# Performance work log

Hardware: AMD Instinct MI355X
Metric: run time of the kernel (lower is better)

## Reference

```python
import math
import jax, jax.numpy as jnp
import numpy as np

N, QLEN, KLEN, DMODEL, NHEAD = 2, 2048, 2048, 1024, 16
DK = DMODEL // NHEAD
MY_INF = 1000000000000.0


def setup_inputs() -> dict:
    key = jax.random.key(0)
    ks = jax.random.split(key, 12)
    s = 1.0 / math.sqrt(DMODEL)
    return {
        "q": jax.random.normal(ks[0], (N, QLEN, DMODEL), jnp.float32),
        "k": jax.random.normal(ks[1], (N, KLEN, DMODEL), jnp.float32),
        "v": jax.random.normal(ks[2], (N, KLEN, DMODEL), jnp.float32),
        "mask": jax.random.randint(ks[3], (N, 1, QLEN, KLEN), 0, 2) > 0,
        "Wq": jax.random.uniform(ks[4], (DMODEL, DMODEL), jnp.float32, -s, s),
        "bq": jnp.zeros((DMODEL,), jnp.float32),
        "Wk": jax.random.uniform(ks[5], (DMODEL, DMODEL), jnp.float32, -s, s),
        "bk": jnp.zeros((DMODEL,), jnp.float32),
        "Wv": jax.random.uniform(ks[6], (DMODEL, DMODEL), jnp.float32, -s, s),
        "bv": jnp.zeros((DMODEL,), jnp.float32),
        "Wo": jax.random.uniform(ks[7], (DMODEL, DMODEL), jnp.float32, -s, s),
        "bo": jnp.zeros((DMODEL,), jnp.float32),
    }


def _mha(q, k, v, mask, Wq, bq, Wk, bk, Wv, bv, Wo, bo):
    n, q_len, _ = q.shape
    k_len = k.shape[1]
    # QKV projections, split into heads: [n, H, len, d_k]
    q_ = (q @ Wq.T + bq).reshape(n, q_len, NHEAD, DK).transpose(0, 2, 1, 3)
    k_ = (k @ Wk.T + bk).reshape(n, k_len, NHEAD, DK).transpose(0, 2, 1, 3)
    v_ = (v @ Wv.T + bv).reshape(n, k_len, NHEAD, DK).transpose(0, 2, 1, 3)
    # scores: [n, H, q_len, k_len]
    scores = jnp.einsum("nhqd,nhkd->nhqk", q_, k_) / math.sqrt(DK)
    scores = jnp.where(mask, -MY_INF, scores)
    attn = jax.nn.softmax(scores, axis=-1)
    ctx = jnp.einsum("nhqk,nhkd->nhqd", attn, v_)
    concat = ctx.transpose(0, 2, 1, 3).reshape(n, q_len, DMODEL)
    # dropout is identity in eval mode
    return concat @ Wo.T + bo


def reference(q, k, v, mask, Wq, bq, Wk, bk, Wv, bv, Wo, bo):
    return _mha(q, k, v, mask, Wq, bq, Wk, bk, Wv, bv, Wo, bo)
```

## Files before the change

kernel.cpp:

```cpp
#include <hip/hip_runtime.h>
#include <hip/hip_bf16.h>
#include <stdint.h>

typedef unsigned short u16;
typedef unsigned long long u64;
typedef __attribute__((ext_vector_type(8))) short bf16x8;
typedef __attribute__((ext_vector_type(4))) float f32x4;

#define DMODEL 1024
#define NHEAD  16
#define DKH    64
#define SEQ    2048
#define NTOK   4096

#define E_QB   0u
#define E_KB   4194304u
#define E_VB   8388608u
#define E_WQ   12582912u
#define E_WK   13631488u
#define E_WV   14680064u
#define E_WO   15728640u
#define E_QP   16777216u
#define E_KP   20971520u
#define E_VT   25165824u
#define E_CTX  4194304u
#define MB_BYTEOFF 0ull

#define MFMA16(a, b, c) __builtin_amdgcn_mfma_f32_16x16x32_bf16(a, b, c, 0, 0, 0)

#define QSCALE (0.125f * 1.4426950408889634f)

__device__ __forceinline__ u16 f2bf(float f) {
  union { float f; uint32_t u; } v; v.f = f;
  uint32_t r = v.u + 0x7fffu + ((v.u >> 16) & 1u);
  return (u16)(r >> 16);
}

__device__ __forceinline__ uint32_t pk_bf16(float a, float b) {
  union { __hip_bfloat162 h; uint32_t u; } c;
  c.h = __float22bfloat162_rn(make_float2(a, b));
  return c.u;
}

__device__ __forceinline__ void gload16(const void* g, void* l) {
  __builtin_amdgcn_global_load_lds(
      (const __attribute__((address_space(1))) unsigned int*)g,
      (__attribute__((address_space(3))) unsigned int*)l, 16, 0, 0);
}

__global__ void convert_k(const float* __restrict__ q, const float* __restrict__ k,
                          const float* __restrict__ v, const float* __restrict__ Wq,
                          const float* __restrict__ Wk, const float* __restrict__ Wv,
                          const float* __restrict__ Wo, u16* __restrict__ ws) {
  const int y = blockIdx.y;
  const float* src;
  int sel = y >> 2;
  if (sel == 0)      src = q + ((size_t)y << 20);
  else if (sel == 1) src = k + ((size_t)(y - 4) << 20);
  else if (sel == 2) src = v + ((size_t)(y - 8) << 20);
  else {
    int wsel = y & 3;
    src = (wsel == 0) ? Wq : (wsel == 1) ? Wk : (wsel == 2) ? Wv : Wo;
  }
  u16* dst = ws + ((size_t)y << 20);
  uint32_t off = blockIdx.x * 256 + threadIdx.x;
#pragma unroll 8
  for (int i = 0; i < 8; ++i, off += 32768) {
    float4 f = ((const float4*)src)[off];
    uint2 o;
    o.x = pk_bf16(f.x, f.y);
    o.y = pk_bf16(f.z, f.w);
    ((uint2*)dst)[off] = o;
  }
}

__global__ void maskbits_k(const int* __restrict__ mask, u64* __restrict__ mb) {
  int wv   = (int)((blockIdx.x * blockDim.x + threadIdx.x) >> 6);
  int lane = threadIdx.x & 63;
#pragma unroll 4
  for (int j = 0; j < 16; ++j) {
    uint32_t w = (uint32_t)wv * 16u + (uint32_t)j;
    int m = mask[(size_t)w * 64 + lane];
    u64 b = __ballot(m != 0);
    if (lane == 0) mb[w] = b;
  }
}

__device__ __forceinline__ void gemm_stage(const u16* A, const u16* B, int bm0, int bn0,
                                           char* smem, int buf, int kt, int tid) {
#pragma unroll
  for (int i = 0; i < 2; ++i) {
    int c = tid + i * 256;
    int row = c >> 2, ko = (c & 3) << 3;
    gload16(A + (size_t)(bm0 + row) * DMODEL + kt * 32 + ko, smem + buf * 16384 + c * 16);
  }
#pragma unroll
  for (int i = 0; i < 2; ++i) {
    int c = tid + i * 256;
    int row = c >> 2, ko = (c & 3) << 3;
    gload16(B + (size_t)(bn0 + row) * DMODEL + kt * 32 + ko,
            smem + buf * 16384 + 8192 + c * 16);
  }
}

__device__ __forceinline__ void gemm_core(const u16* A, const u16* B, int bm0, int bn0,
                                          char* smem, f32x4 (&acc)[4][4]) {
  const int tid = threadIdx.x;
  const int lane = tid & 63, w = tid >> 6;
  const int wr = w >> 1, wc = w & 1;
  const int low = lane & 15, g = lane >> 4;

  gemm_stage(A, B, bm0, bn0, smem, 0, 0, tid);
  for (int kt = 0; kt < 32; ++kt) {
    const int cur = kt & 1;
    __syncthreads();
    if (kt + 1 < 32) gemm_stage(A, B, bm0, bn0, smem, cur ^ 1, kt + 1, tid);
    const char* As = smem + cur * 16384;
    const char* Bs = As + 8192;
    bf16x8 av[4], bv8[4];
#pragma unroll
    for (int m = 0; m < 4; ++m)
      av[m] = *(const bf16x8*)(As + ((wr * 64 + m * 16 + low) * 32 + g * 8) * 2);
#pragma unroll
    for (int n = 0; n < 4; ++n)
      bv8[n] = *(const bf16x8*)(Bs + ((wc * 64 + n * 16 + low) * 32 + g * 8) * 2);
    __builtin_amdgcn_s_setprio(1);
#pragma unroll
    for (int m = 0; m < 4; ++m)
#pragma unroll
      for (int n = 0; n < 4; ++n)
        acc[m][n] = MFMA16(av[m], bv8[n], acc[m][n]);
    __builtin_amdgcn_s_setprio(0);
  }
}

__global__ __launch_bounds__(256) void qkv_gemm_k(const u16* __restrict__ wsr,
                                                  u16* __restrict__ wsw,
                                                  const float* __restrict__ bq,
                                                  const float* __restrict__ bk,
                                                  const float* __restrict__ bv) {
  __shared__ char smem[35328];
  int linear = blockIdx.x + (blockIdx.y << 3) + (blockIdx.z << 8);
  int sw = (linear & 7) * 96 + (linear >> 3);
  const int z = sw >> 8;
  const int bm0 = ((sw >> 3) & 31) * 128, bn0 = (sw & 7) * 128;
  const u16* A = wsr + (z == 0 ? E_QB : z == 1 ? E_KB : E_VB);
  const u16* B = wsr + (z == 0 ? E_WQ : z == 1 ? E_WK : E_WV);
  const float* bias = (z == 0) ? bq : (z == 1) ? bk : bv;
  const float scale = (z == 0) ? QSCALE : 1.0f;

  f32x4 acc[4][4] = {};
  gemm_core(A, B, bm0, bn0, smem, acc);

  const int tid = threadIdx.x, lane = tid & 63, w = tid >> 6;
  const int wr = w >> 1, wc = w & 1, low = lane & 15, g = lane >> 4;

  const int pitch = (z == 2) ? 138 : 136;

  __syncthreads();
  u16* eps = (u16*)smem;
#pragma unroll
  for (int n = 0; n < 4; ++n) {
    float bn_ = bias[bn0 + wc * 64 + n * 16 + low];
#pragma unroll
    for (int m = 0; m < 4; ++m)
#pragma unroll
      for (int r = 0; r < 4; ++r) {
        int row = wr * 64 + m * 16 + g * 4 + r;
        int col = wc * 64 + n * 16 + low;
        eps[row * pitch + col] = f2bf((acc[m][n][r] + bn_) * scale);
      }
  }
  __syncthreads();

  if (z < 2) {
    u16* dst = wsw + (z == 0 ? E_QP : E_KP);
#pragma unroll
    for (int i = 0; i < 8; ++i) {
      int c = tid + i * 256;
      int row = c >> 4, seg = c & 15;
      bf16x8 vv = *(const bf16x8*)(eps + row * 136 + seg * 8);
      int token = bm0 + row, nb_ = token >> 11, t = token & 2047;
      int od = bn0 + seg * 8, h = od >> 6, d = od & 63;
      *(bf16x8*)(dst + (((size_t)(nb_ * NHEAD + h) * SEQ + t) << 6) + d) = vv;
    }
  } else {
    u16* dst = wsw + E_VT;
#pragma unroll
    for (int i = 0; i < 8; ++i) {
      int c = tid + i * 256;
      int col = c >> 4, r0 = (c & 15) << 3;
      bf16x8 vv;
#pragma unroll
      for (int j = 0; j < 8; ++j) vv[j] = (short)eps[(r0 + j) * 138 + col];
      int od = bn0 + col, h = od >> 6, d = od & 63;
      int token0 = bm0 + r0, nb_ = token0 >> 11, t0 = token0 & 2047;
      *(bf16x8*)(dst + ((size_t)((nb_ * NHEAD + h) * DKH + d) << 11) + t0) = vv;
    }
  }
}

__global__ __launch_bounds__(256, 4) void attn_k(const u16* __restrict__ ws,
                                                 u16* __restrict__ wsw,
                                                 const u64* __restrict__ mb) {
  __shared__ char smem[40960];
  int linear = blockIdx.x + (blockIdx.y << 5);
  int sw = (linear & 7) * 128 + (linear >> 3);
  const int qt = sw & 31;
  const int nh = sw >> 5;
  const int n_ = nh >> 4, h = nh & 15;
  const int tid = threadIdx.x, lane = tid & 63, w = tid >> 6;
  const int low = lane & 15, g = lane >> 4;

  const u16* Qp = ws + E_QP + ((size_t)nh * SEQ << 6);
  const u16* Kp = ws + E_KP + ((size_t)nh * SEQ << 6);
  const u16* VT = ws + E_VT + ((size_t)nh * DKH << 11);
  const u64* mbase = mb + (size_t)n_ * SEQ * 32;
  const int qrow0 = qt * 64 + w * 16;

  bf16x8 aq[2];
#pragma unroll
  for (int ks = 0; ks < 2; ++ks)
    aq[ks] = *(const bf16x8*)(Qp + ((size_t)(qrow0 + low) << 6) + ks * 32 + g * 8);

  float lsum[4] = {0.f, 0.f, 0.f, 0.f};
  f32x4 o[4] = {};

  u16* Ps = (u16*)(smem + 32768) + w * 16 * 64;

#define STAGE_KV(buf, kv0)                                                        \
  {                                                                               \
    _Pragma("unroll") for (int i = 0; i < 2; ++i) {                               \
      int c = tid + i * 256;                                                      \
      int row = c >> 3, cc = c & 7, sc = cc ^ (row & 7);                          \
      gload16(Kp + ((size_t)((kv0) + row) << 6) + sc * 8, smem + (buf) * 8192 + c * 16); \
    }                                                                             \
    _Pragma("unroll") for (int i = 0; i < 2; ++i) {                               \
      int c = tid + i * 256;                                                      \
      int row = c >> 3, cc = c & 7, sc = cc ^ (row & 7);                          \
      gload16(VT + ((size_t)row << 11) + (kv0) + sc * 8,                          \
              smem + 16384 + (buf) * 8192 + c * 16);                              \
    }                                                                             \
  }

  STAGE_KV(0, 0)
  for (int it = 0; it < 32; ++it) {
    const int cur = it & 1;
    const int kv0 = it << 6;
    __syncthreads();
    if (it + 1 < 32) STAGE_KV(cur ^ 1, kv0 + 64)

    f32x4 s[4] = {};
    const char* Ksb = smem + cur * 8192;
#pragma unroll
    for (int ks = 0; ks < 2; ++ks) {
      bf16x8 bk8[4];
#pragma unroll
      for (int cf = 0; cf < 4; ++cf) {
        int rk = cf * 16 + low;
        bk8[cf] = *(const bf16x8*)(Ksb + rk * 128 + (((ks << 2) + g) ^ (low & 7)) * 16);
      }
      __builtin_amdgcn_s_setprio(1);
#pragma unroll
      for (int cf = 0; cf < 4; ++cf) s[cf] = MFMA16(aq[ks], bk8[cf], s[cf]);
      __builtin_amdgcn_s_setprio(0);
    }

#pragma unroll
    for (int r = 0; r < 4; ++r) {
      int qrow = qrow0 + g * 4 + r;
      u64 mw = mbase[(size_t)qrow * 32 + it];
      uint32_t mlo = (uint32_t)mw, mhi = (uint32_t)(mw >> 32);
      float p0 = exp2f(s[0][r]);
      float p1 = exp2f(s[1][r]);
      float p2 = exp2f(s[2][r]);
      float p3 = exp2f(s[3][r]);
      if ((mlo >> low) & 1u) p0 = 0.0f;
      if ((mlo >> (low + 16)) & 1u) p1 = 0.0f;
      if ((mhi >> low) & 1u) p2 = 0.0f;
      if ((mhi >> (low + 16)) & 1u) p3 = 0.0f;
      lsum[r] += (p0 + p1) + (p2 + p3);
      uint32_t u01 = pk_bf16(p0, p1);
      uint32_t u23 = pk_bf16(p2, p3);
      int prow = g * 4 + r;
      int swz = prow & 7, lo3 = low & 7, hi1 = low >> 3;
      u16* Pr = Ps + prow * 64 + lo3;
      Pr[(((0 * 2 + hi1) ^ swz) << 3)] = (u16)u01;
      Pr[(((1 * 2 + hi1) ^ swz) << 3)] = (u16)(u01 >> 16);
      Pr[(((2 * 2 + hi1) ^ swz) << 3)] = (u16)u23;
      Pr[(((3 * 2 + hi1) ^ swz) << 3)] = (u16)(u23 >> 16);
    }
    asm volatile("s_waitcnt lgkmcnt(0)" ::: "memory");
    __builtin_amdgcn_sched_barrier(0);

    const char* Vsb = smem + 16384 + cur * 8192;
#pragma unroll
    for (int ks = 0; ks < 2; ++ks) {
      bf16x8 ap = *(const bf16x8*)((const char*)Ps + low * 128 +
                                   ((((ks << 2) + g) ^ (low & 7)) << 4));
      bf16x8 bvv[4];
#pragma unroll
      for (int df = 0; df < 4; ++df) {
        int rv = df * 16 + low;
        bvv[df] = *(const bf16x8*)(Vsb + rv * 128 + (((ks << 2) + g) ^ (low & 7)) * 16);
      }
      __builtin_amdgcn_s_setprio(1);
#pragma unroll
      for (int df = 0; df < 4; ++df) o[df] = MFMA16(ap, bvv[df], o[df]);
      __builtin_amdgcn_s_setprio(0);
    }
  }

  float inv[4];
#pragma unroll
  for (int r = 0; r < 4; ++r) {
    float ls = lsum[r];
    ls += __shfl_xor(ls, 1);
    ls += __shfl_xor(ls, 2);
    ls += __shfl_xor(ls, 4);
    ls += __shfl_xor(ls, 8);
    inv[r] = 1.0f / ls;
  }

#pragma unroll
  for (int r = 0; r < 4; ++r) {
    int prow = g * 4 + r;
    int swz = prow & 7, lo3 = low & 7, hi1 = low >> 3;
    u16* Pr = Ps + prow * 64 + lo3;
#pragma unroll
    for (int df = 0; df < 4; ++df)
      Pr[(((df * 2 + hi1) ^ swz) << 3)] = f2bf(o[df][r] * inv[r]);
  }
  asm volatile("s_waitcnt lgkmcnt(0)" ::: "memory");
  __builtin_amdgcn_sched_barrier(0);
  u16* ctx = wsw + E_CTX;
#pragma unroll
  for (int j = 0; j < 2; ++j) {
    int c = lane + j * 64;
    int row = c >> 3, seg = c & 7;
    bf16x8 vv = *(const bf16x8*)((const char*)Ps + row * 128 +
                                 ((seg ^ (row & 7)) << 4));
    int token = qt * 64 + w * 16 + row;
    *(bf16x8*)(ctx + ((size_t)(n_ * SEQ + token) << 10) + h * 64 + seg * 8) = vv;
  }
#undef STAGE_KV
}

__global__ __launch_bounds__(256) void outproj_k(const u16* __restrict__ ws,
                                                 const float* __restrict__ bo,
                                                 float* __restrict__ out) {
  __shared__ char smem[32768];
  int linear = blockIdx.x + (blockIdx.y << 3);
  int sw = (linear & 7) * 32 + (linear >> 3);
  const int bm0 = (sw >> 3) * 128, bn0 = (sw & 7) * 128;
  const u16* A = ws + E_CTX;
  const u16* B = ws + E_WO;

  f32x4 acc[4][4] = {};
  gemm_core(A, B, bm0, bn0, smem, acc);

  const int tid = threadIdx.x, lane = tid & 63, w = tid >> 6;
  const int wr = w >> 1, wc = w & 1, low = lane & 15, g = lane >> 4;
#pragma unroll
  for (int n = 0; n < 4; ++n) {
    float b = bo[bn0 + wc * 64 + n * 16 + low];
    int col = bn0 + wc * 64 + n * 16 + low;
#pragma unroll
    for (int m = 0; m < 4; ++m)
#pragma unroll
      for (int r = 0; r < 4; ++r) {
        int row = bm0 + wr * 64 + m * 16 + g * 4 + r;
        out[(size_t)row * DMODEL + col] = acc[m][n][r] + b;
      }
  }
}

extern "C" void kernel_launch(void* const* d_in, const int* in_sizes, int n_in,
                              void* d_out, int out_size, void* d_ws, size_t ws_size,
                              hipStream_t stream) {
  const float* q  = (const float*)d_in[0];
  const float* k  = (const float*)d_in[1];
  const float* v  = (const float*)d_in[2];
  const int* mask = (const int*)d_in[3];
  const float* Wq = (const float*)d_in[4];
  const float* bq = (const float*)d_in[5];
  const float* Wk = (const float*)d_in[6];
  const float* bk = (const float*)d_in[7];
  const float* Wv = (const float*)d_in[8];
  const float* bv = (const float*)d_in[9];
  const float* Wo = (const float*)d_in[10];
  const float* bo = (const float*)d_in[11];
  float* out = (float*)d_out;
  u16* ws = (u16*)d_ws;
  u64* mb = (u64*)((char*)d_ws + MB_BYTEOFF);

  convert_k<<<dim3(128, 16), dim3(256), 0, stream>>>(q, k, v, Wq, Wk, Wv, Wo, ws);
  qkv_gemm_k<<<dim3(8, 32, 3), dim3(256), 0, stream>>>(ws, ws, bq, bk, bv);
  maskbits_k<<<dim3(2048), dim3(256), 0, stream>>>(mask, mb);
  attn_k<<<dim3(32, 32), dim3(256), 0, stream>>>(ws, ws, mb);
  outproj_k<<<dim3(8, 32), dim3(256), 0, stream>>>(ws, bo, out);
}
```

Measured before the change: 276.5 us.

## Give each attention wave two 16-row Q tiles with transposed S computation

The attention kernel now runs 2 waves of 128 threads per block, each wave owning 32 query rows (two MFMA M-fragments), so every K/V fragment loaded from LDS feeds two MFMAs. S is computed transposed (K as the A operand), which lets each lane read one 64-bit mask word per row and write packed P with 8-byte stores. The row-sum reduction becomes a cross-group shuffle, and exp2f is replaced by the raw v_exp_f32 builtin. Register pressure and per-block staging work per thread both rise, and the launch bound falls to 128 threads with min 2 blocks, which may reduce occupancy.

```diff
diff --git a/kernel.cpp b/kernel.cpp
--- a/kernel.cpp
+++ b/kernel.cpp
@@ -29,6 +29,16 @@
 #define MFMA16(a, b, c) __builtin_amdgcn_mfma_f32_16x16x32_bf16(a, b, c, 0, 0, 0)
 
 #define QSCALE (0.125f * 1.4426950408889634f)
+
+__device__ __forceinline__ float exp2_fast(float x) {
+#if __has_builtin(__builtin_amdgcn_exp2f)
+  return __builtin_amdgcn_exp2f(x);
+#else
+  float r;
+  asm("v_exp_f32 %0, %1" : "=v"(r) : "v"(x));
+  return r;
+#endif
+}
 
 __device__ __forceinline__ u16 f2bf(float f) {
   union { float f; uint32_t u; } v; v.f = f;
@@ -200,7 +210,7 @@
   }
 }
 
-__global__ __launch_bounds__(256, 4) void attn_k(const u16* __restrict__ ws,
+__global__ __launch_bounds__(128, 2) void attn_k(const u16* __restrict__ ws,
                                                  u16* __restrict__ wsw,
                                                  const u64* __restrict__ mb) {
   __shared__ char smem[40960];
@@ -211,32 +221,35 @@
   const int n_ = nh >> 4, h = nh & 15;
   const int tid = threadIdx.x, lane = tid & 63, w = tid >> 6;
   const int low = lane & 15, g = lane >> 4;
+  const int e = (low & 7) << 1;
 
   const u16* Qp = ws + E_QP + ((size_t)nh * SEQ << 6);
   const u16* Kp = ws + E_KP + ((size_t)nh * SEQ << 6);
   const u16* VT = ws + E_VT + ((size_t)nh * DKH << 11);
   const u64* mbase = mb + (size_t)n_ * SEQ * 32;
-  const int qrow0 = qt * 64 + w * 16;
-
-  bf16x8 aq[2];
-#pragma unroll
-  for (int ks = 0; ks < 2; ++ks)
-    aq[ks] = *(const bf16x8*)(Qp + ((size_t)(qrow0 + low) << 6) + ks * 32 + g * 8);
-
-  float lsum[4] = {0.f, 0.f, 0.f, 0.f};
-  f32x4 o[4] = {};
-
-  u16* Ps = (u16*)(smem + 32768) + w * 16 * 64;
+  const int qrow0 = qt * 64 + w * 32;
+
+  bf16x8 aq[2][2];
+#pragma unroll
+  for (int mf = 0; mf < 2; ++mf)
+#pragma unroll
+    for (int ks = 0; ks < 2; ++ks)
+      aq[mf][ks] = *(const bf16x8*)(Qp + ((size_t)(qrow0 + mf * 16 + low) << 6) +
+                                    ks * 32 + g * 8);
+
+  float lsum[2] = {0.f, 0.f};
+  f32x4 o[2][4] = {};
+  char* Pw = smem + 32768 + w * 4096;
 
 #define STAGE_KV(buf, kv0)                                                        \
   {                                                                               \
-    _Pragma("unroll") for (int i = 0; i < 2; ++i) {                               \
-      int c = tid + i * 256;                                                      \
+    _Pragma("unroll") for (int i = 0; i < 4; ++i) {                               \
+      int c = tid + i * 128;                                                      \
       int row = c >> 3, cc = c & 7, sc = cc ^ (row & 7);                          \
       gload16(Kp + ((size_t)((kv0) + row) << 6) + sc * 8, smem + (buf) * 8192 + c * 16); \
     }                                                                             \
-    _Pragma("unroll") for (int i = 0; i < 2; ++i) {                               \
-      int c = tid + i * 256;                                                      \
+    _Pragma("unroll") for (int i = 0; i < 4; ++i) {                               \
+      int c = tid + i * 128;                                                      \
       int row = c >> 3, cc = c & 7, sc = cc ^ (row & 7);                          \
       gload16(VT + ((size_t)row << 11) + (kv0) + sc * 8,                          \
               smem + 16384 + (buf) * 8192 + c * 16);                              \
@@ -250,7 +263,7 @@
     __syncthreads();
     if (it + 1 < 32) STAGE_KV(cur ^ 1, kv0 + 64)
 
-    f32x4 s[4] = {};
+    f32x4 st[2][4] = {};
     const char* Ksb = smem + cur * 8192;
 #pragma unroll
     for (int ks = 0; ks < 2; ++ks) {
@@ -260,35 +273,35 @@
         int rk = cf * 16 + low;
         bk8[cf] = *(const bf16x8*)(Ksb + rk * 128 + (((ks << 2) + g) ^ (low & 7)) * 16);
       }
-      __builtin_amdgcn_s_setprio(1);
-#pragma unroll
-      for (int cf = 0; cf < 4; ++cf) s[cf] = MFMA16(aq[ks], bk8[cf], s[cf]);
-      __builtin_amdgcn_s_setprio(0);
-    }
-
-#pragma unroll
-    for (int r = 0; r < 4; ++r) {
-      int qrow = qrow0 + g * 4 + r;
-      u64 mw = mbase[(size_t)qrow * 32 + it];
-      uint32_t mlo = (uint32_t)mw, mhi = (uint32_t)(mw >> 32);
-      float p0 = exp2f(s[0][r]);
-      float p1 = exp2f(s[1][r]);
-      float p2 = exp2f(s[2][r]);
-      float p3 = exp2f(s[3][r]);
-      if ((mlo >> low) & 1u) p0 = 0.0f;
-      if ((mlo >> (low + 16)) & 1u) p1 = 0.0f;
-      if ((mhi >> low) & 1u) p2 = 0.0f;
-      if ((mhi >> (low + 16)) & 1u) p3 = 0.0f;
-      lsum[r] += (p0 + p1) + (p2 + p3);
-      uint32_t u01 = pk_bf16(p0, p1);
-      uint32_t u23 = pk_bf16(p2, p3);
-      int prow = g * 4 + r;
-      int swz = prow & 7, lo3 = low & 7, hi1 = low >> 3;
-      u16* Pr = Ps + prow * 64 + lo3;
-      Pr[(((0 * 2 + hi1) ^ swz) << 3)] = (u16)u01;
-      Pr[(((1 * 2 + hi1) ^ swz) << 3)] = (u16)(u01 >> 16);
-      Pr[(((2 * 2 + hi1) ^ swz) << 3)] = (u16)u23;
-      Pr[(((3 * 2 + hi1) ^ swz) << 3)] = (u16)(u23 >> 16);
+#pragma unroll
+      for (int mf = 0; mf < 2; ++mf)
+#pragma unroll
+        for (int cf = 0; cf < 4; ++cf)
+          st[mf][cf] = MFMA16(bk8[cf], aq[mf][ks], st[mf][cf]);
+    }
+
+#pragma unroll
+    for (int mf = 0; mf < 2; ++mf) {
+      u64 mw = mbase[(size_t)(qrow0 + mf * 16 + low) * 32 + it];
+      float ls = 0.f;
+#pragma unroll
+      for (int cf = 0; cf < 4; ++cf) {
+        uint32_t mb4 = (uint32_t)(mw >> (cf * 16 + g * 4));
+        float p0 = exp2_fast(st[mf][cf][0]);
+        float p1 = exp2_fast(st[mf][cf][1]);
+        float p2 = exp2_fast(st[mf][cf][2]);
+        float p3 = exp2_fast(st[mf][cf][3]);
+        if (mb4 & 1u) p0 = 0.0f;
+        if (mb4 & 2u) p1 = 0.0f;
+        if (mb4 & 4u) p2 = 0.0f;
+        if (mb4 & 8u) p3 = 0.0f;
+        ls += (p0 + p1) + (p2 + p3);
+        uint2 pr;
+        pr.x = pk_bf16(p0, p1);
+        pr.y = pk_bf16(p2, p3);
+        *(uint2*)(Pw + (mf * 16 + low) * 128 + ((((cf << 2) | g) ^ e) << 3)) = pr;
+      }
+      lsum[mf] += ls;
     }
     asm volatile("s_waitcnt lgkmcnt(0)" ::: "memory");
     __builtin_amdgcn_sched_barrier(0);
@@ -296,51 +309,57 @@
     const char* Vsb = smem + 16384 + cur * 8192;
 #pragma unroll
     for (int ks = 0; ks < 2; ++ks) {
-      bf16x8 ap = *(const bf16x8*)((const char*)Ps + low * 128 +
-                                   ((((ks << 2) + g) ^ (low & 7)) << 4));
+      int pc = (((ks << 3) | (g << 1)) ^ e) << 3;
+      bf16x8 ap0 = *(const bf16x8*)(Pw + low * 128 + pc);
+      bf16x8 ap1 = *(const bf16x8*)(Pw + (16 + low) * 128 + pc);
       bf16x8 bvv[4];
 #pragma unroll
       for (int df = 0; df < 4; ++df) {
         int rv = df * 16 + low;
         bvv[df] = *(const bf16x8*)(Vsb + rv * 128 + (((ks << 2) + g) ^ (low & 7)) * 16);
       }
-      __builtin_amdgcn_s_setprio(1);
-#pragma unroll
-      for (int df = 0; df < 4; ++df) o[df] = MFMA16(ap, bvv[df], o[df]);
-      __builtin_amdgcn_s_setprio(0);
-    }
-  }
-
-  float inv[4];
-#pragma unroll
-  for (int r = 0; r < 4; ++r) {
-    float ls = lsum[r];
-    ls += __shfl_xor(ls, 1);
-    ls += __shfl_xor(ls, 2);
-    ls += __shfl_xor(ls, 4);
-    ls += __shfl_xor(ls, 8);
-    inv[r] = 1.0f / ls;
-  }
-
-#pragma unroll
-  for (int r = 0; r < 4; ++r) {
-    int prow = g * 4 + r;
-    int swz = prow & 7, lo3 = low & 7, hi1 = low >> 3;
-    u16* Pr = Ps + prow * 64 + lo3;
-#pragma unroll
-    for (int df = 0; df < 4; ++df)
-      Pr[(((df * 2 + hi1) ^ swz) << 3)] = f2bf(o[df][r] * inv[r]);
-  }
+#pragma unroll
+      for (int df = 0; df < 4; ++df) {
+        o[0][df] = MFMA16(ap0, bvv[df], o[0][df]);
+        o[1][df] = MFMA16(ap1, bvv[df], o[1][df]);
+      }
+    }
+  }
+
+  float invr[2][4];
+#pragma unroll
+  for (int mf = 0; mf < 2; ++mf) {
+    float ls = lsum[mf];
+    ls += __shfl_xor(ls, 16);
+    ls += __shfl_xor(ls, 32);
+    float inv = 1.0f / ls;
+#pragma unroll
+    for (int r = 0; r < 4; ++r)
+      invr[mf][r] = __shfl(inv, g * 4 + r);
+  }
+
+#pragma unroll
+  for (int mf = 0; mf < 2; ++mf)
+#pragma unroll
+    for (int df = 0; df < 4; ++df) {
+      int c8 = (df << 2) | (low >> 2);
+#pragma unroll
+      for (int r = 0; r < 4; ++r) {
+        int row = mf * 16 + g * 4 + r;
+        int e2 = (row & 7) << 1;
+        *(u16*)(Pw + row * 128 + ((c8 ^ e2) << 3) + ((low & 3) << 1)) =
+            f2bf(o[mf][df][r] * invr[mf][r]);
+      }
+    }
   asm volatile("s_waitcnt lgkmcnt(0)" ::: "memory");
   __builtin_amdgcn_sched_barrier(0);
   u16* ctx = wsw + E_CTX;
 #pragma unroll
-  for (int j = 0; j < 2; ++j) {
+  for (int j = 0; j < 4; ++j) {
     int c = lane + j * 64;
     int row = c >> 3, seg = c & 7;
-    bf16x8 vv = *(const bf16x8*)((const char*)Ps + row * 128 +
-                                 ((seg ^ (row & 7)) << 4));
-    int token = qt * 64 + w * 16 + row;
+    bf16x8 vv = *(const bf16x8*)(Pw + row * 128 + ((seg ^ (row & 7)) << 4));
+    int token = qt * 64 + w * 32 + row;
     *(bf16x8*)(ctx + ((size_t)(n_ * SEQ + token) << 10) + h * 64 + seg * 8) = vv;
   }
 #undef STAGE_KV
@@ -397,6 +416,6 @@
   convert_k<<<dim3(128, 16), dim3(256), 0, stream>>>(q, k, v, Wq, Wk, Wv, Wo, ws);
   qkv_gemm_k<<<dim3(8, 32, 3), dim3(256), 0, stream>>>(ws, ws, bq, bk, bv);
   maskbits_k<<<dim3(2048), dim3(256), 0, stream>>>(mask, mb);
-  attn_k<<<dim3(32, 32), dim3(256), 0, stream>>>(ws, ws, mb);
+  attn_k<<<dim3(32, 32), dim3(128), 0, stream>>>(ws, ws, mb);
   outproj_k<<<dim3(8, 32), dim3(256), 0, stream>>>(ws, bo, out);
 }
```

Measured after the change: 269.1 us. 1.03x faster.
